# Performance work log

Hardware: AMD Instinct MI355X
Metric: run time of the kernel (lower is better)

Reference implementation:

```python
import jax, jax.numpy as jnp
import numpy as np

EMB = 1024
FF = 4 * EMB

def _ternary(w):
    # BitNet b1.58 absmean quantization; forward uses pure ternary weights
    scale = jnp.maximum(jnp.mean(jnp.abs(w)), 1e-8)
    w_t = jnp.clip(jnp.round(w / scale), -1.0, 1.0)
    # STE: forward = w_t, backward = identity w.r.t. w
    return w + jax.lax.stop_gradient(w_t - w)

def setup_inputs() -> dict:
    key = jax.random.key(0)
    kx, k1, k2, kb1, kb2 = jax.random.split(key, 5)
    x = jax.random.normal(kx, (4, 2048, EMB), dtype=jnp.float32)
    # nn.Linear default init: U(-1/sqrt(fan_in), 1/sqrt(fan_in))
    lim1 = 1.0 / np.sqrt(EMB)
    lim2 = 1.0 / np.sqrt(FF)
    W1 = jax.random.uniform(k1, (FF, EMB), jnp.float32, -lim1, lim1)
    b1 = jax.random.uniform(kb1, (FF,), jnp.float32, -lim1, lim1)
    W2 = jax.random.uniform(k2, (EMB, FF), jnp.float32, -lim2, lim2)
    b2 = jax.random.uniform(kb2, (EMB,), jnp.float32, -lim2, lim2)
    return {"x": x, "W1": W1, "b1": b1, "W2": W2, "b2": b2}

def reference(x, W1, b1, W2, b2):
    h = jnp.einsum('bsd,fd->bsf', x, _ternary(W1)) + b1  # [B,S,FF]
    h = jax.nn.gelu(h, approximate=False)  # torch nn.GELU default = exact erf
    out = jnp.einsum('bsf,df->bsd', h, _ternary(W2)) + b2  # [B,S,EMB]
    return out
```

## Files before the change

### kernel.cpp

```cpp
#include <hip/hip_runtime.h>
#include <hip/hip_bf16.h>
#include <cstdint>
#include <cstddef>

typedef __bf16 bf16x8 __attribute__((ext_vector_type(8)));
typedef float  f32x4  __attribute__((ext_vector_type(4)));

__device__ __forceinline__ unsigned short f2bf(float f) {
    __hip_bfloat16 b = __float2bfloat16(f);
    return *reinterpret_cast<unsigned short*>(&b);
}

__device__ __forceinline__ float fast_gelu(float x) {
    float x2 = x * x;
    float m  = x * __builtin_fmaf(x2, -0.10294314f, -2.30220795f);
    float e  = __builtin_amdgcn_exp2f(m);
    return x * __builtin_amdgcn_rcpf(1.0f + e);
}


__global__ void abs_sum_cvt_kernel(const float4* __restrict__ w0, const float4* __restrict__ w1,
                                   int n4w, float* __restrict__ part,
                                   const float4* __restrict__ x, ushort4* __restrict__ xb,
                                   int n4x) {
    int seg = (int)blockIdx.x >> 9;
    int b = (int)blockIdx.x & 511;
    if (seg == 2) {
        for (int i = b * blockDim.x + threadIdx.x; i < n4x; i += 512 * blockDim.x) {
            float4 v = x[i];
            ushort4 o;
            o.x = f2bf(v.x); o.y = f2bf(v.y); o.z = f2bf(v.z); o.w = f2bf(v.w);
            xb[i] = o;
        }
        return;
    }
    const float4* w = seg ? w1 : w0;
    float s = 0.0f;
    for (int i = b * blockDim.x + threadIdx.x; i < n4w; i += 512 * blockDim.x) {
        float4 v = w[i];
        s += fabsf(v.x) + fabsf(v.y) + fabsf(v.z) + fabsf(v.w);
    }
    #pragma unroll
    for (int o = 32; o > 0; o >>= 1) s += __shfl_down(s, o, 64);
    __shared__ float ps[4];
    int lane = threadIdx.x & 63, wid = threadIdx.x >> 6;
    if (lane == 0) ps[wid] = s;
    __syncthreads();
    if (threadIdx.x == 0) part[blockIdx.x] = ps[0] + ps[1] + ps[2] + ps[3];
}

__global__ void ternarize_kernel(const float4* __restrict__ w0, ushort4* __restrict__ t0,
                                 const float4* __restrict__ w1, ushort4* __restrict__ t1,
                                 int n4w, const float* __restrict__ part, float inv_n) {
    int seg = (int)blockIdx.x >> 10;
    int b = (int)blockIdx.x & 1023;

    float s = 0.0f;
    for (int j = threadIdx.x; j < 512; j += 256) s += part[seg * 512 + j];
    #pragma unroll
    for (int o = 32; o > 0; o >>= 1) s += __shfl_down(s, o, 64);
    __shared__ float ps[4];
    __shared__ float sscale;
    int lane = threadIdx.x & 63, wid = threadIdx.x >> 6;
    if (lane == 0) ps[wid] = s;
    __syncthreads();
    if (threadIdx.x == 0) {
        float tot = ps[0] + ps[1] + ps[2] + ps[3];
        sscale = fmaxf(tot * inv_n, 1e-8f);
    }
    __syncthreads();
    float inv = 1.0f / sscale;

    const float4* w = seg ? w1 : w0;
    ushort4* t = seg ? t1 : t0;
    for (int i = b * blockDim.x + threadIdx.x; i < n4w; i += 1024 * blockDim.x) {
        float4 v = w[i];
        ushort4 o;
        o.x = f2bf(fminf(fmaxf(rintf(v.x * inv), -1.0f), 1.0f));
        o.y = f2bf(fminf(fmaxf(rintf(v.y * inv), -1.0f), 1.0f));
        o.z = f2bf(fminf(fmaxf(rintf(v.z * inv), -1.0f), 1.0f));
        o.w = f2bf(fminf(fmaxf(rintf(v.w * inv), -1.0f), 1.0f));
        t[i] = o;
    }
}


template <int EPI, int K, int N>
__global__ __launch_bounds__(256)
void gemm_bt_kernel(const unsigned short* __restrict__ A,
                    const unsigned short* __restrict__ B,
                    const float* __restrict__ bias,
                    void* __restrict__ C) {
    __shared__ __align__(16) unsigned short As[128 * 64];
    __shared__ __align__(16) unsigned short Bs[128 * 64];

    const int tid  = threadIdx.x;
    const int lane = tid & 63;
    const int wid  = tid >> 6;
    const int mBase = (wid >> 1) * 64;
    const int nBase = (wid & 1) * 64;
    const int lr = lane & 15;
    const int lq = lane >> 4;

    const size_t aRow0 = (size_t)blockIdx.y * 128;
    const size_t bRow0 = (size_t)blockIdx.x * 128;

    const int rA  = tid >> 3;
    const int cSw = (((tid & 7) ^ (rA & 7)) << 3);
    const unsigned short* ga = A + (aRow0 + rA) * (size_t)K + cSw;
    const unsigned short* gb = B + (bRow0 + rA) * (size_t)K + cSw;
    unsigned short* ldsA = &As[tid * 8];
    unsigned short* ldsB = &Bs[tid * 8];

    f32x4 acc[4][4];
    #pragma unroll
    for (int i = 0; i < 4; ++i)
        #pragma unroll
        for (int j = 0; j < 4; ++j)
            acc[i][j] = f32x4{0.f, 0.f, 0.f, 0.f};

    const int swz0 = ((lq ^ (lr & 7)) << 3);
    const int swz1 = (((4 + lq) ^ (lr & 7)) << 3);

    #pragma unroll 2
    for (int k0 = 0; k0 < K; k0 += 64) {
        __syncthreads();
        #pragma unroll
        for (int t = 0; t < 4; ++t) {
            __builtin_amdgcn_global_load_lds(
                (const __attribute__((address_space(1))) void*)(ga + (size_t)t * 32 * K),
                (__attribute__((address_space(3))) void*)(ldsA + t * 2048), 16, 0, 0);
            __builtin_amdgcn_global_load_lds(
                (const __attribute__((address_space(1))) void*)(gb + (size_t)t * 32 * K),
                (__attribute__((address_space(3))) void*)(ldsB + t * 2048), 16, 0, 0);
        }
        ga += 64;
        gb += 64;
        __syncthreads();
        #pragma unroll
        for (int ks = 0; ks < 2; ++ks) {
            const int swz = ks ? swz1 : swz0;
            bf16x8 avec[4], bvec[4];
            #pragma unroll
            for (int i = 0; i < 4; ++i) {
                avec[i] = *(const bf16x8*)&As[(mBase + i * 16 + lr) * 64 + swz];
                bvec[i] = *(const bf16x8*)&Bs[(nBase + i * 16 + lr) * 64 + swz];
            }
            #pragma unroll
            for (int mi = 0; mi < 4; ++mi)
                #pragma unroll
                for (int ni = 0; ni < 4; ++ni)
                    acc[mi][ni] = __builtin_amdgcn_mfma_f32_16x16x32_bf16(
                        avec[mi], bvec[ni], acc[mi][ni], 0, 0, 0);
        }
    }

    #pragma unroll
    for (int mi = 0; mi < 4; ++mi) {
        #pragma unroll
        for (int ni = 0; ni < 4; ++ni) {
            int col = (int)bRow0 + nBase + ni * 16 + lr;
            float bv = bias[col];
            #pragma unroll
            for (int r = 0; r < 4; ++r) {
                size_t row = aRow0 + mBase + mi * 16 + lq * 4 + r;
                float v = acc[mi][ni][r] + bv;
                if (EPI == 0) {
                    ((unsigned short*)C)[row * (size_t)N + col] = f2bf(fast_gelu(v));
                } else {
                    ((float*)C)[row * (size_t)N + col] = v;
                }
            }
        }
    }
}


extern "C" void kernel_launch(void* const* d_in, const int* in_sizes, int n_in,
                              void* d_out, int out_size, void* d_ws, size_t ws_size,
                              hipStream_t stream) {
    const float* x  = (const float*)d_in[0];
    const float* W1 = (const float*)d_in[1];
    const float* b1 = (const float*)d_in[2];
    const float* W2 = (const float*)d_in[3];
    const float* b2 = (const float*)d_in[4];
    float* out = (float*)d_out;

    const int M = 8192, EMB = 1024, FF = 4096;
    const int nW = FF * EMB;

    char* ws = (char*)d_ws;
    float* part = (float*)ws;
    unsigned short* W1t = (unsigned short*)(ws + 16384);
    unsigned short* W2t = W1t + (size_t)nW;
    unsigned short* xb  = W2t + (size_t)nW;
    unsigned short* h   = xb  + (size_t)M * EMB;

    abs_sum_cvt_kernel<<<1536, 256, 0, stream>>>((const float4*)W1, (const float4*)W2,
                                                 nW / 4, part,
                                                 (const float4*)x, (ushort4*)xb,
                                                 (M * EMB) / 4);
    ternarize_kernel<<<2048, 256, 0, stream>>>((const float4*)W1, (ushort4*)W1t,
                                               (const float4*)W2, (ushort4*)W2t,
                                               nW / 4, part, 1.0f / nW);

    gemm_bt_kernel<0, 1024, 4096><<<dim3(FF / 128, M / 128), 256, 0, stream>>>(xb, W1t, b1, h);
    gemm_bt_kernel<1, 4096, 1024><<<dim3(EMB / 128, M / 128), 256, 0, stream>>>(h, W2t, b2, out);
}
```

Baseline: 268.7 us.

## Fuse quantization and both GEMMs into one persistent kernel with grid barriers

Replaces the four kernel launches with a single persistent kernel of 768 blocks. Software grid barriers built on atomic counters separate four phases: abs-sum, ternarize plus the rest of the x conversion, GEMM1, and GEMM2. The aim is to remove launch gaps and tail effects between stages. In exchange it needs all 768 blocks co-resident (launch bounds of 3 blocks per CU), a memset of the counters, and spin-wait barriers. GEMM2 now runs on only 512 of the 768 blocks, and GEMM1 tiles are distributed round-robin, leaving an uneven last wave.

```diff
diff --git a/kernel.cpp b/kernel.cpp
--- a/kernel.cpp
+++ b/kernel.cpp
@@ -18,82 +18,23 @@
     return x * __builtin_amdgcn_rcpf(1.0f + e);
 }
 
-
-__global__ void abs_sum_cvt_kernel(const float4* __restrict__ w0, const float4* __restrict__ w1,
-                                   int n4w, float* __restrict__ part,
-                                   const float4* __restrict__ x, ushort4* __restrict__ xb,
-                                   int n4x) {
-    int seg = (int)blockIdx.x >> 9;
-    int b = (int)blockIdx.x & 511;
-    if (seg == 2) {
-        for (int i = b * blockDim.x + threadIdx.x; i < n4x; i += 512 * blockDim.x) {
-            float4 v = x[i];
-            ushort4 o;
-            o.x = f2bf(v.x); o.y = f2bf(v.y); o.z = f2bf(v.z); o.w = f2bf(v.w);
-            xb[i] = o;
-        }
-        return;
-    }
-    const float4* w = seg ? w1 : w0;
-    float s = 0.0f;
-    for (int i = b * blockDim.x + threadIdx.x; i < n4w; i += 512 * blockDim.x) {
-        float4 v = w[i];
-        s += fabsf(v.x) + fabsf(v.y) + fabsf(v.z) + fabsf(v.w);
-    }
-    #pragma unroll
-    for (int o = 32; o > 0; o >>= 1) s += __shfl_down(s, o, 64);
-    __shared__ float ps[4];
-    int lane = threadIdx.x & 63, wid = threadIdx.x >> 6;
-    if (lane == 0) ps[wid] = s;
-    __syncthreads();
-    if (threadIdx.x == 0) part[blockIdx.x] = ps[0] + ps[1] + ps[2] + ps[3];
-}
-
-__global__ void ternarize_kernel(const float4* __restrict__ w0, ushort4* __restrict__ t0,
-                                 const float4* __restrict__ w1, ushort4* __restrict__ t1,
-                                 int n4w, const float* __restrict__ part, float inv_n) {
-    int seg = (int)blockIdx.x >> 10;
-    int b = (int)blockIdx.x & 1023;
-
-    float s = 0.0f;
-    for (int j = threadIdx.x; j < 512; j += 256) s += part[seg * 512 + j];
-    #pragma unroll
-    for (int o = 32; o > 0; o >>= 1) s += __shfl_down(s, o, 64);
-    __shared__ float ps[4];
-    __shared__ float sscale;
-    int lane = threadIdx.x & 63, wid = threadIdx.x >> 6;
-    if (lane == 0) ps[wid] = s;
+__device__ __forceinline__ void grid_bar(unsigned* ctr, unsigned target) {
     __syncthreads();
     if (threadIdx.x == 0) {
-        float tot = ps[0] + ps[1] + ps[2] + ps[3];
-        sscale = fmaxf(tot * inv_n, 1e-8f);
+        __hip_atomic_fetch_add(ctr, 1u, __ATOMIC_ACQ_REL, __HIP_MEMORY_SCOPE_AGENT);
+        while (__hip_atomic_load(ctr, __ATOMIC_ACQUIRE, __HIP_MEMORY_SCOPE_AGENT) < target)
+            __builtin_amdgcn_s_sleep(1);
     }
     __syncthreads();
-    float inv = 1.0f / sscale;
-
-    const float4* w = seg ? w1 : w0;
-    ushort4* t = seg ? t1 : t0;
-    for (int i = b * blockDim.x + threadIdx.x; i < n4w; i += 1024 * blockDim.x) {
-        float4 v = w[i];
-        ushort4 o;
-        o.x = f2bf(fminf(fmaxf(rintf(v.x * inv), -1.0f), 1.0f));
-        o.y = f2bf(fminf(fmaxf(rintf(v.y * inv), -1.0f), 1.0f));
-        o.z = f2bf(fminf(fmaxf(rintf(v.z * inv), -1.0f), 1.0f));
-        o.w = f2bf(fminf(fmaxf(rintf(v.w * inv), -1.0f), 1.0f));
-        t[i] = o;
-    }
-}
-
+}
 
 template <int EPI, int K, int N>
-__global__ __launch_bounds__(256)
-void gemm_bt_kernel(const unsigned short* __restrict__ A,
-                    const unsigned short* __restrict__ B,
-                    const float* __restrict__ bias,
-                    void* __restrict__ C) {
-    __shared__ __align__(16) unsigned short As[128 * 64];
-    __shared__ __align__(16) unsigned short Bs[128 * 64];
-
+__device__ __forceinline__ void gemm_tile(const unsigned short* __restrict__ A,
+                                          const unsigned short* __restrict__ B,
+                                          const float* __restrict__ bias,
+                                          void* __restrict__ C,
+                                          int bx, int by,
+                                          unsigned short* As, unsigned short* Bs) {
     const int tid  = threadIdx.x;
     const int lane = tid & 63;
     const int wid  = tid >> 6;
@@ -102,15 +43,15 @@
     const int lr = lane & 15;
     const int lq = lane >> 4;
 
-    const size_t aRow0 = (size_t)blockIdx.y * 128;
-    const size_t bRow0 = (size_t)blockIdx.x * 128;
+    const size_t aRow0 = (size_t)by * 128;
+    const size_t bRow0 = (size_t)bx * 128;
 
     const int rA  = tid >> 3;
     const int cSw = (((tid & 7) ^ (rA & 7)) << 3);
     const unsigned short* ga = A + (aRow0 + rA) * (size_t)K + cSw;
     const unsigned short* gb = B + (bRow0 + rA) * (size_t)K + cSw;
-    unsigned short* ldsA = &As[tid * 8];
-    unsigned short* ldsB = &Bs[tid * 8];
+    unsigned short* ldsA = As + tid * 8;
+    unsigned short* ldsB = Bs + tid * 8;
 
     f32x4 acc[4][4];
     #pragma unroll
@@ -173,6 +114,103 @@
             }
         }
     }
+}
+
+__global__ __launch_bounds__(256, 3)
+void ffn_fused_kernel(const float* __restrict__ x,
+                      const float* __restrict__ W1, const float* __restrict__ b1,
+                      const float* __restrict__ W2, const float* __restrict__ b2,
+                      float* __restrict__ out,
+                      unsigned* __restrict__ ctr,
+                      float* __restrict__ part,
+                      unsigned short* __restrict__ W1t,
+                      unsigned short* __restrict__ W2t,
+                      unsigned short* __restrict__ xb,
+                      unsigned short* __restrict__ h) {
+    __shared__ __align__(16) unsigned short As[128 * 64];
+    __shared__ __align__(16) unsigned short Bs[128 * 64];
+    __shared__ float ps[4];
+    __shared__ float sscale;
+
+    const int bid = blockIdx.x;
+    const int tid = threadIdx.x;
+    const int lane = tid & 63, wv = tid >> 6;
+
+    const int N4W = 1 << 20;
+    const int N4X = 1 << 21;
+    const int XHALF = 1 << 20;
+
+    {
+        int seg = bid >> 8;
+        int b = bid & 255;
+        if (seg < 2) {
+            const float4* w = (const float4*)(seg ? W2 : W1);
+            float s = 0.0f;
+            for (int i = b * 256 + tid; i < N4W; i += 256 * 256) {
+                float4 v = w[i];
+                s += fabsf(v.x) + fabsf(v.y) + fabsf(v.z) + fabsf(v.w);
+            }
+            #pragma unroll
+            for (int o = 32; o > 0; o >>= 1) s += __shfl_down(s, o, 64);
+            if (lane == 0) ps[wv] = s;
+            __syncthreads();
+            if (tid == 0) part[bid] = ps[0] + ps[1] + ps[2] + ps[3];
+        } else {
+            const float4* xf = (const float4*)x;
+            ushort4* xo = (ushort4*)xb;
+            for (int i = b * 256 + tid; i < XHALF; i += 256 * 256) {
+                float4 v = xf[i];
+                ushort4 o;
+                o.x = f2bf(v.x); o.y = f2bf(v.y); o.z = f2bf(v.z); o.w = f2bf(v.w);
+                xo[i] = o;
+            }
+        }
+    }
+    grid_bar(&ctr[0], 768u);
+
+    {
+        int seg = (bid < 384) ? 0 : 1;
+        float s = part[seg * 256 + tid];
+        #pragma unroll
+        for (int o = 32; o > 0; o >>= 1) s += __shfl_down(s, o, 64);
+        __syncthreads();
+        if (lane == 0) ps[wv] = s;
+        __syncthreads();
+        if (tid == 0)
+            sscale = fmaxf((ps[0] + ps[1] + ps[2] + ps[3]) * (1.0f / 4194304.0f), 1e-8f);
+        __syncthreads();
+        float inv = 1.0f / sscale;
+
+        int b = seg ? (bid - 384) : bid;
+        const float4* w = (const float4*)(seg ? W2 : W1);
+        ushort4* t = seg ? (ushort4*)W2t : (ushort4*)W1t;
+        for (int i = b * 256 + tid; i < N4W; i += 384 * 256) {
+            float4 v = w[i];
+            ushort4 o;
+            o.x = f2bf(fminf(fmaxf(rintf(v.x * inv), -1.0f), 1.0f));
+            o.y = f2bf(fminf(fmaxf(rintf(v.y * inv), -1.0f), 1.0f));
+            o.z = f2bf(fminf(fmaxf(rintf(v.z * inv), -1.0f), 1.0f));
+            o.w = f2bf(fminf(fmaxf(rintf(v.w * inv), -1.0f), 1.0f));
+            t[i] = o;
+        }
+        const float4* xf = (const float4*)x;
+        ushort4* xo = (ushort4*)xb;
+        for (int i = XHALF + bid * 256 + tid; i < N4X; i += 768 * 256) {
+            float4 v = xf[i];
+            ushort4 o;
+            o.x = f2bf(v.x); o.y = f2bf(v.y); o.z = f2bf(v.z); o.w = f2bf(v.w);
+            xo[i] = o;
+        }
+    }
+    grid_bar(&ctr[1], 768u);
+
+    #pragma unroll 1
+    for (int t = bid; t < 2048; t += 768)
+        gemm_tile<0, 1024, 4096>(xb, W1t, b1, h, t & 31, t >> 5, As, Bs);
+    grid_bar(&ctr[2], 768u);
+
+    if (bid < 512)
+        gemm_tile<1, 4096, 1024>(h, W2t, b2, out, bid & 7, bid >> 3, As, Bs);
 }
 
 
@@ -186,24 +224,19 @@
     const float* b2 = (const float*)d_in[4];
     float* out = (float*)d_out;
 
-    const int M = 8192, EMB = 1024, FF = 4096;
-    const int nW = FF * EMB;
+    const size_t nW = 4096ull * 1024ull;
+    const size_t nX = 8192ull * 1024ull;
 
     char* ws = (char*)d_ws;
-    float* part = (float*)ws;
+    unsigned* ctr = (unsigned*)ws;
+    float* part = (float*)(ws + 256);
     unsigned short* W1t = (unsigned short*)(ws + 16384);
-    unsigned short* W2t = W1t + (size_t)nW;
-    unsigned short* xb  = W2t + (size_t)nW;
-    unsigned short* h   = xb  + (size_t)M * EMB;
-
-    abs_sum_cvt_kernel<<<1536, 256, 0, stream>>>((const float4*)W1, (const float4*)W2,
-                                                 nW / 4, part,
-                                                 (const float4*)x, (ushort4*)xb,
-                                                 (M * EMB) / 4);
-    ternarize_kernel<<<2048, 256, 0, stream>>>((const float4*)W1, (ushort4*)W1t,
-                                               (const float4*)W2, (ushort4*)W2t,
-                                               nW / 4, part, 1.0f / nW);
-
-    gemm_bt_kernel<0, 1024, 4096><<<dim3(FF / 128, M / 128), 256, 0, stream>>>(xb, W1t, b1, h);
-    gemm_bt_kernel<1, 4096, 1024><<<dim3(EMB / 128, M / 128), 256, 0, stream>>>(h, W2t, b2, out);
-}
+    unsigned short* W2t = W1t + nW;
+    unsigned short* xb  = W2t + nW;
+    unsigned short* h   = xb + nX;
+
+    hipMemsetAsync(ctr, 0, 256, stream);
+
+    ffn_fused_kernel<<<dim3(768), dim3(256), 0, stream>>>(
+        x, W1, b1, W2, b2, out, ctr, part, W1t, W2t, xb, h);
+}
```

After: 495.9 us. +84.5%, slower.
